# Kernel optimization log

Hardware: AMD Instinct MI355X
Metric: run time of the kernel (lower is better)

## Reference

```python
import jax, jax.numpy as jnp
import numpy as np

E, IN, H1, H2, H3, A, B = 20, 512, 1024, 512, 256, 32, 4096


def setup_inputs() -> dict:
    key = jax.random.key(0)
    ks = jax.random.split(key, 10)

    def w(k, shape, fan_in):
        return jax.random.normal(k, shape, dtype=jnp.float32) / np.sqrt(fan_in)

    return {
        "obs": jax.random.normal(ks[0], (B, IN), dtype=jnp.float32),
        # stacked expert MLP params [E, ...]
        "eW1": w(ks[1], (E, IN, H1), IN), "eb1": jnp.zeros((E, H1), jnp.float32),
        "eW2": w(ks[2], (E, H1, H2), H1), "eb2": jnp.zeros((E, H2), jnp.float32),
        "eW3": w(ks[3], (E, H2, H3), H2), "eb3": jnp.zeros((E, H3), jnp.float32),
        "eW4": w(ks[4], (E, H3, A), H3), "eb4": jnp.zeros((E, A), jnp.float32),
        # gate MLP params
        "gW1": w(ks[5], (IN, H1), IN), "gb1": jnp.zeros((H1,), jnp.float32),
        "gW2": w(ks[6], (H1, H2), H1), "gb2": jnp.zeros((H2,), jnp.float32),
        "gW3": w(ks[7], (H2, H3), H2), "gb3": jnp.zeros((H3,), jnp.float32),
        "gW4": w(ks[8], (H3, E), H3), "gb4": jnp.zeros((E,), jnp.float32),
    }


def _experts(obs, eW1, eb1, eW2, eb2, eW3, eb3, eW4, eb4):
    # batched over experts: [B, E, h]
    h = jax.nn.elu(jnp.einsum('bi,eih->beh', obs, eW1) + eb1[None])
    h = jax.nn.elu(jnp.einsum('beh,ehk->bek', h, eW2) + eb2[None])
    h = jax.nn.elu(jnp.einsum('bek,ekm->bem', h, eW3) + eb3[None])
    return jnp.einsum('bem,ema->bea', h, eW4) + eb4[None]  # [B, E, A]


def _gate(obs, gW1, gb1, gW2, gb2, gW3, gb3, gW4, gb4):
    h = jax.nn.elu(obs @ gW1 + gb1)
    h = jax.nn.elu(h @ gW2 + gb2)
    h = jax.nn.elu(h @ gW3 + gb3)
    return jax.nn.softmax(h @ gW4 + gb4, axis=-1)  # [B, E]


def reference(obs, eW1, eb1, eW2, eb2, eW3, eb3, eW4, eb4,
              gW1, gb1, gW2, gb2, gW3, gb3, gW4, gb4):
    weights = _gate(obs, gW1, gb1, gW2, gb2, gW3, gb3, gW4, gb4)       # [B, E]
    actions = _experts(obs, eW1, eb1, eW2, eb2, eW3, eb3, eW4, eb4)    # [B, E, A]
    # bmm(weights[:,None,:], actions).squeeze(1)
    return jnp.einsum('be,bea->ba', weights, actions)                   # [B, A]
```

## Files before the change

### kernel.cpp

```cpp
#include <hip/hip_runtime.h>

#define B_SZ 4096
#define E_EXP 20
#define NE 21

typedef unsigned short u16;
typedef __bf16 bf16x8 __attribute__((ext_vector_type(8)));
typedef u16 u16x8 __attribute__((ext_vector_type(8)));
typedef u16 u16x4 __attribute__((ext_vector_type(4)));
typedef float floatx4 __attribute__((ext_vector_type(4)));

static __device__ __forceinline__ u16 f2bf(float f) {
  unsigned u = __builtin_bit_cast(unsigned, f);
  u += 0x7fffu + ((u >> 16) & 1u);
  return (u16)(u >> 16);
}

static __device__ __forceinline__ bf16x8 ld_bf8(const u16* p) {
  u16x8 v = *reinterpret_cast<const u16x8*>(p);
  return __builtin_bit_cast(bf16x8, v);
}

static __device__ __forceinline__ void gld_lds16(const u16* g, u16* l) {
  __builtin_amdgcn_global_load_lds(
      (const __attribute__((address_space(1))) unsigned int*)g,
      (__attribute__((address_space(3))) unsigned int*)l, 16, 0, 0);
}


__global__ void convert_obs_kernel(const float* __restrict__ src,
                                   u16* __restrict__ dst, int n) {
  int i = (blockIdx.x * blockDim.x + threadIdx.x) * 4;
  if (i < n) {
    float4 v = *reinterpret_cast<const float4*>(src + i);
    u16x4 o;
    o.x = f2bf(v.x); o.y = f2bf(v.y); o.z = f2bf(v.z); o.w = f2bf(v.w);
    *reinterpret_cast<u16x4*>(dst + i) = o;
  }
}

__global__ void transpose_conv_kernel(const float* __restrict__ src_e,
                                      const float* __restrict__ src_g,
                                      int n_e, int K, int N, int Nout,
                                      u16* __restrict__ dst) {
  int e = blockIdx.z;
  const float* src = (e < n_e) ? (src_e + (long)e * K * N) : src_g;
  __shared__ float tile[32][33];
  int tx = threadIdx.x & 31;
  int ty = threadIdx.x >> 5;
  int kbase = blockIdx.x * 32;
  int nbase = blockIdx.y * 32;
#pragma unroll
  for (int i = 0; i < 4; ++i) {
    int k = kbase + ty + i * 8;
    int n = nbase + tx;
    float v = 0.f;
    if (k < K && n < N) v = src[(long)k * N + n];
    tile[ty + i * 8][tx] = v;
  }
  __syncthreads();
  u16* dstE = dst + (long)e * Nout * K;
#pragma unroll
  for (int i = 0; i < 4; ++i) {
    int n = nbase + ty + i * 8;
    int k = kbase + tx;
    if (n < Nout && k < K) dstE[(long)n * K + k] = f2bf(tile[tx][ty + i * 8]);
  }
}

__global__ void concat_bias_kernel(const float* __restrict__ e_b,
                                   const float* __restrict__ g_b,
                                   int E, int H, float* __restrict__ dst) {
  int i = blockIdx.x * blockDim.x + threadIdx.x;
  int total = (E + 1) * H;
  if (i < total) dst[i] = (i < E * H) ? e_b[i] : g_b[i - E * H];
}


#define BM 128
#define BN 128
#define BK 32

__global__ __launch_bounds__(256) void gemm_bias_elu_kernel(
    const u16* __restrict__ A_base, long a_estride,
    const u16* __restrict__ Wt_base, long w_estride,
    const float* __restrict__ bias_base, long b_estride,
    u16* __restrict__ C_base, long c_estride,
    int M, int N, int K) {
  int e = blockIdx.z;
  const u16* A = A_base + (long)e * a_estride;
  const u16* Wt = Wt_base + (long)e * w_estride;
  const float* bias = bias_base + (long)e * b_estride;
  u16* C = C_base + (long)e * c_estride;

  int m0 = blockIdx.y * BM;
  int n0 = blockIdx.x * BN;

  __shared__ u16 As[BM * BK];
  __shared__ u16 Bs[BN * BK];

  int tid = threadIdx.x;
  int lane = tid & 63;
  int w = tid >> 6;
  int wm = (w >> 1) * 64;
  int wn = (w & 1) * 64;
  int col = lane & 15;
  int quad = lane >> 4;

  floatx4 acc[4][4] = {};

  int srow = tid >> 2;
  int scol = (tid & 3) * 8;
  const u16* ga0 = &A[(long)(m0 + srow) * K + scol];
  const u16* ga1 = &A[(long)(m0 + 64 + srow) * K + scol];
  const u16* gb0 = &Wt[(long)(n0 + srow) * K + scol];
  const u16* gb1 = &Wt[(long)(n0 + 64 + srow) * K + scol];
  u16* la0 = &As[(size_t)tid * 8];
  u16* la1 = &As[(size_t)(256 + tid) * 8];
  u16* lb0 = &Bs[(size_t)tid * 8];
  u16* lb1 = &Bs[(size_t)(256 + tid) * 8];

  for (int k0 = 0; k0 < K; k0 += BK) {
    __syncthreads();
    gld_lds16(ga0 + k0, la0);
    gld_lds16(ga1 + k0, la1);
    gld_lds16(gb0 + k0, lb0);
    gld_lds16(gb1 + k0, lb1);
    __syncthreads();

    bf16x8 af[4], bfr[4];
#pragma unroll
    for (int t = 0; t < 4; ++t) {
      af[t] = __builtin_bit_cast(bf16x8,
          *reinterpret_cast<u16x8*>(&As[(wm + t * 16 + col) * BK + quad * 8]));
      bfr[t] = __builtin_bit_cast(bf16x8,
          *reinterpret_cast<u16x8*>(&Bs[(wn + t * 16 + col) * BK + quad * 8]));
    }
#pragma unroll
    for (int i = 0; i < 4; ++i)
#pragma unroll
      for (int j = 0; j < 4; ++j)
        acc[i][j] = __builtin_amdgcn_mfma_f32_16x16x32_bf16(af[i], bfr[j],
                                                            acc[i][j], 0, 0, 0);
  }

#pragma unroll
  for (int i = 0; i < 4; ++i) {
    int row = m0 + wm + i * 16 + quad * 4;
#pragma unroll
    for (int j = 0; j < 4; ++j) {
      int c = n0 + wn + j * 16 + col;
      float bj = bias[c];
#pragma unroll
      for (int r = 0; r < 4; ++r) {
        float v = acc[i][j][r] + bj;
        v = v > 0.f ? v : (__expf(v) - 1.f);
        C[(long)(row + r) * N + c] = f2bf(v);
      }
    }
  }
}

__global__ __launch_bounds__(64) void final_combine_kernel(
    const u16* __restrict__ h3, const u16* __restrict__ W4t,
    const u16* __restrict__ gW4t, const float* __restrict__ eb4,
    const float* __restrict__ gb4, float* __restrict__ out) {
  const int H3 = 256;
  int lane = threadIdx.x;
  int col = lane & 15;
  int quad = lane >> 4;
  int r0 = blockIdx.x * 16;

  floatx4 g0 = {}, g1 = {};
  const u16* h3g = h3 + (long)E_EXP * B_SZ * H3;
#pragma unroll
  for (int k0 = 0; k0 < 256; k0 += 32) {
    bf16x8 a = ld_bf8(&h3g[(long)(r0 + col) * H3 + k0 + quad * 8]);
    bf16x8 b0 = ld_bf8(&gW4t[(long)col * H3 + k0 + quad * 8]);
    bf16x8 b1 = ld_bf8(&gW4t[(long)(16 + col) * H3 + k0 + quad * 8]);
    g0 = __builtin_amdgcn_mfma_f32_16x16x32_bf16(a, b0, g0, 0, 0, 0);
    g1 = __builtin_amdgcn_mfma_f32_16x16x32_bf16(a, b1, g1, 0, 0, 0);
  }

  float w0[4], w1[4];
  float gbc0 = gb4[col];
  float gbc1 = (col < 4) ? gb4[16 + col] : 0.f;
#pragma unroll
  for (int r = 0; r < 4; ++r) {
    float v0 = g0[r] + gbc0;
    float v1 = (col < 4) ? (g1[r] + gbc1) : -1e30f;
    float m = fmaxf(v0, v1);
#pragma unroll
    for (int s = 1; s < 16; s <<= 1) m = fmaxf(m, __shfl_xor(m, s, 64));
    float e0 = __expf(v0 - m);
    float e1 = (col < 4) ? __expf(v1 - m) : 0.f;
    float ssum = e0 + e1;
#pragma unroll
    for (int s = 1; s < 16; s <<= 1) ssum += __shfl_xor(ssum, s, 64);
    w0[r] = e0 / ssum;
    w1[r] = e1 / ssum;
  }

  floatx4 o0 = {}, o1 = {};
  for (int e = 0; e < E_EXP; ++e) {
    floatx4 a0 = {}, a1 = {};
    const u16* he = h3 + (long)e * B_SZ * H3;
    const u16* we = W4t + (long)e * 32 * H3;
#pragma unroll
    for (int k0 = 0; k0 < 256; k0 += 32) {
      bf16x8 a = ld_bf8(&he[(long)(r0 + col) * H3 + k0 + quad * 8]);
      bf16x8 b0 = ld_bf8(&we[(long)col * H3 + k0 + quad * 8]);
      bf16x8 b1 = ld_bf8(&we[(long)(16 + col) * H3 + k0 + quad * 8]);
      a0 = __builtin_amdgcn_mfma_f32_16x16x32_bf16(a, b0, a0, 0, 0, 0);
      a1 = __builtin_amdgcn_mfma_f32_16x16x32_bf16(a, b1, a1, 0, 0, 0);
    }
    float be0 = eb4[e * 32 + col];
    float be1 = eb4[e * 32 + 16 + col];
    int src = (lane & 48) + (e & 15);
#pragma unroll
    for (int r = 0; r < 4; ++r) {
      float wr = __shfl((e < 16) ? w0[r] : w1[r], src, 64);
      o0[r] += wr * (a0[r] + be0);
      o1[r] += wr * (a1[r] + be1);
    }
  }
#pragma unroll
  for (int r = 0; r < 4; ++r) {
    int row = r0 + quad * 4 + r;
    out[(long)row * 32 + col] = o0[r];
    out[(long)row * 32 + 16 + col] = o1[r];
  }
}


static inline size_t align256(size_t x) { return (x + 255) & ~(size_t)255; }

extern "C" void kernel_launch(void* const* d_in, const int* in_sizes, int n_in,
                              void* d_out, int out_size, void* d_ws,
                              size_t ws_size, hipStream_t stream) {
  const float* obs = (const float*)d_in[0];
  const float* eW1 = (const float*)d_in[1];
  const float* eb1 = (const float*)d_in[2];
  const float* eW2 = (const float*)d_in[3];
  const float* eb2 = (const float*)d_in[4];
  const float* eW3 = (const float*)d_in[5];
  const float* eb3 = (const float*)d_in[6];
  const float* eW4 = (const float*)d_in[7];
  const float* eb4 = (const float*)d_in[8];
  const float* gW1 = (const float*)d_in[9];
  const float* gb1 = (const float*)d_in[10];
  const float* gW2 = (const float*)d_in[11];
  const float* gb2 = (const float*)d_in[12];
  const float* gW3 = (const float*)d_in[13];
  const float* gb3 = (const float*)d_in[14];
  const float* gW4 = (const float*)d_in[15];
  const float* gb4 = (const float*)d_in[16];
  float* out = (float*)d_out;
  char* ws = (char*)d_ws;

  size_t off = 0;
  size_t OFF_OBS = off;  off = align256(off + (size_t)B_SZ * 512 * 2);
  size_t OFF_W1T = off;  off = align256(off + (size_t)NE * 1024 * 512 * 2);
  size_t OFF_W2T = off;  off = align256(off + (size_t)NE * 512 * 1024 * 2);
  size_t OFF_W3T = off;  off = align256(off + (size_t)NE * 256 * 512 * 2);
  size_t OFF_W4T = off;  off = align256(off + (size_t)E_EXP * 32 * 256 * 2);
  size_t OFF_GW4T = off; off = align256(off + (size_t)32 * 256 * 2);
  size_t OFF_B1 = off;   off = align256(off + (size_t)NE * 1024 * 4);
  size_t OFF_B2 = off;   off = align256(off + (size_t)NE * 512 * 4);
  size_t OFF_B3 = off;   off = align256(off + (size_t)NE * 256 * 4);
  size_t OFF_H3 = off;   off = align256(off + (size_t)NE * B_SZ * 256 * 2);

  int chunk = B_SZ;
  size_t OFF_H1 = off;
  while (chunk > 512) {
    size_t need = (size_t)NE * chunk * 1024 * 2 + (size_t)NE * chunk * 512 * 2;
    if (OFF_H1 + need <= ws_size) break;
    chunk >>= 1;
  }
  size_t OFF_H2 = align256(OFF_H1 + (size_t)NE * chunk * 1024 * 2);

  u16* obs_bf = (u16*)(ws + OFF_OBS);
  u16* W1t = (u16*)(ws + OFF_W1T);
  u16* W2t = (u16*)(ws + OFF_W2T);
  u16* W3t = (u16*)(ws + OFF_W3T);
  u16* W4t = (u16*)(ws + OFF_W4T);
  u16* gW4t = (u16*)(ws + OFF_GW4T);
  float* b1 = (float*)(ws + OFF_B1);
  float* b2 = (float*)(ws + OFF_B2);
  float* b3 = (float*)(ws + OFF_B3);
  u16* h3 = (u16*)(ws + OFF_H3);
  u16* h1 = (u16*)(ws + OFF_H1);
  u16* h2 = (u16*)(ws + OFF_H2);

  convert_obs_kernel<<<(B_SZ * 512 / 4 + 255) / 256, 256, 0, stream>>>(
      obs, obs_bf, B_SZ * 512);
  transpose_conv_kernel<<<dim3(16, 32, NE), 256, 0, stream>>>(
      eW1, gW1, E_EXP, 512, 1024, 1024, W1t);
  transpose_conv_kernel<<<dim3(32, 16, NE), 256, 0, stream>>>(
      eW2, gW2, E_EXP, 1024, 512, 512, W2t);
  transpose_conv_kernel<<<dim3(16, 8, NE), 256, 0, stream>>>(
      eW3, gW3, E_EXP, 512, 256, 256, W3t);
  transpose_conv_kernel<<<dim3(8, 1, E_EXP), 256, 0, stream>>>(
      eW4, nullptr, E_EXP, 256, 32, 32, W4t);
  transpose_conv_kernel<<<dim3(8, 1, 1), 256, 0, stream>>>(
      gW4, nullptr, 1, 256, 20, 32, gW4t);
  concat_bias_kernel<<<(NE * 1024 + 255) / 256, 256, 0, stream>>>(
      eb1, gb1, E_EXP, 1024, b1);
  concat_bias_kernel<<<(NE * 512 + 255) / 256, 256, 0, stream>>>(
      eb2, gb2, E_EXP, 512, b2);
  concat_bias_kernel<<<(NE * 256 + 255) / 256, 256, 0, stream>>>(
      eb3, gb3, E_EXP, 256, b3);

  for (int bc = 0; bc < B_SZ; bc += chunk) {
    gemm_bias_elu_kernel<<<dim3(1024 / BN, chunk / BM, NE), 256, 0, stream>>>(
        obs_bf + (size_t)bc * 512, 0L,
        W1t, (long)1024 * 512,
        b1, 1024L,
        h1, (long)chunk * 1024, chunk, 1024, 512);
    gemm_bias_elu_kernel<<<dim3(512 / BN, chunk / BM, NE), 256, 0, stream>>>(
        h1, (long)chunk * 1024,
        W2t, (long)512 * 1024,
        b2, 512L,
        h2, (long)chunk * 512, chunk, 512, 1024);
    gemm_bias_elu_kernel<<<dim3(256 / BN, chunk / BM, NE), 256, 0, stream>>>(
        h2, (long)chunk * 512,
        W3t, (long)256 * 512,
        b3, 256L,
        h3 + (size_t)bc * 256, (long)B_SZ * 256, chunk, 256, 512);
  }

  final_combine_kernel<<<B_SZ / 16, 64, 0, stream>>>(h3, W4t, gW4t, eb4, gb4,
                                                     out);
}
```

Baseline: 575.0 us.

## Persist GEMM blocks over M tiles and vectorize transposed bias-ELU epilogue

Each GEMM block now loops over several M tiles (grid y capped at 4 or 8) so the same weight tile rows are re-read by fewer blocks and stay hot in cache. The MFMA operands are swapped so each lane holds four consecutive output columns, which lets the epilogue load the bias as a float4 and store four bf16 values at once instead of scalar strided stores. The cost is fewer blocks in flight, which can leave compute units idle on small chunks.

```diff
diff --git a/kernel.cpp b/kernel.cpp
--- a/kernel.cpp
+++ b/kernel.cpp
@@ -14,6 +14,10 @@
   unsigned u = __builtin_bit_cast(unsigned, f);
   u += 0x7fffu + ((u >> 16) & 1u);
   return (u16)(u >> 16);
+}
+
+static __device__ __forceinline__ float elu1(float v) {
+  return v > 0.f ? v : (__expf(v) - 1.f);
 }
 
 static __device__ __forceinline__ bf16x8 ld_bf8(const u16* p) {
@@ -93,7 +97,6 @@
   const float* bias = bias_base + (long)e * b_estride;
   u16* C = C_base + (long)e * c_estride;
 
-  int m0 = blockIdx.y * BM;
   int n0 = blockIdx.x * BN;
 
   __shared__ u16 As[BM * BK];
@@ -107,12 +110,8 @@
   int col = lane & 15;
   int quad = lane >> 4;
 
-  floatx4 acc[4][4] = {};
-
   int srow = tid >> 2;
   int scol = (tid & 3) * 8;
-  const u16* ga0 = &A[(long)(m0 + srow) * K + scol];
-  const u16* ga1 = &A[(long)(m0 + 64 + srow) * K + scol];
   const u16* gb0 = &Wt[(long)(n0 + srow) * K + scol];
   const u16* gb1 = &Wt[(long)(n0 + 64 + srow) * K + scol];
   u16* la0 = &As[(size_t)tid * 8];
@@ -120,42 +119,51 @@
   u16* lb0 = &Bs[(size_t)tid * 8];
   u16* lb1 = &Bs[(size_t)(256 + tid) * 8];
 
-  for (int k0 = 0; k0 < K; k0 += BK) {
-    __syncthreads();
-    gld_lds16(ga0 + k0, la0);
-    gld_lds16(ga1 + k0, la1);
-    gld_lds16(gb0 + k0, lb0);
-    gld_lds16(gb1 + k0, lb1);
-    __syncthreads();
-
-    bf16x8 af[4], bfr[4];
-#pragma unroll
-    for (int t = 0; t < 4; ++t) {
-      af[t] = __builtin_bit_cast(bf16x8,
-          *reinterpret_cast<u16x8*>(&As[(wm + t * 16 + col) * BK + quad * 8]));
-      bfr[t] = __builtin_bit_cast(bf16x8,
-          *reinterpret_cast<u16x8*>(&Bs[(wn + t * 16 + col) * BK + quad * 8]));
+  int mtiles = M / BM;
+  for (int mt = blockIdx.y; mt < mtiles; mt += gridDim.y) {
+    int m0 = mt * BM;
+    const u16* ga0 = &A[(long)(m0 + srow) * K + scol];
+    const u16* ga1 = &A[(long)(m0 + 64 + srow) * K + scol];
+
+    floatx4 acc[4][4] = {};
+
+    for (int k0 = 0; k0 < K; k0 += BK) {
+      __syncthreads();
+      gld_lds16(ga0 + k0, la0);
+      gld_lds16(ga1 + k0, la1);
+      gld_lds16(gb0 + k0, lb0);
+      gld_lds16(gb1 + k0, lb1);
+      __syncthreads();
+
+      bf16x8 xf[4], wf[4];
+#pragma unroll
+      for (int t = 0; t < 4; ++t) {
+        xf[t] = __builtin_bit_cast(bf16x8,
+            *reinterpret_cast<u16x8*>(&As[(wm + t * 16 + col) * BK + quad * 8]));
+        wf[t] = __builtin_bit_cast(bf16x8,
+            *reinterpret_cast<u16x8*>(&Bs[(wn + t * 16 + col) * BK + quad * 8]));
+      }
+#pragma unroll
+      for (int i = 0; i < 4; ++i)
+#pragma unroll
+        for (int j = 0; j < 4; ++j)
+          acc[i][j] = __builtin_amdgcn_mfma_f32_16x16x32_bf16(
+              wf[j], xf[i], acc[i][j], 0, 0, 0);
     }
-#pragma unroll
-    for (int i = 0; i < 4; ++i)
-#pragma unroll
-      for (int j = 0; j < 4; ++j)
-        acc[i][j] = __builtin_amdgcn_mfma_f32_16x16x32_bf16(af[i], bfr[j],
-                                                            acc[i][j], 0, 0, 0);
-  }
-
-#pragma unroll
-  for (int i = 0; i < 4; ++i) {
-    int row = m0 + wm + i * 16 + quad * 4;
+
 #pragma unroll
     for (int j = 0; j < 4; ++j) {
-      int c = n0 + wn + j * 16 + col;
-      float bj = bias[c];
-#pragma unroll
-      for (int r = 0; r < 4; ++r) {
-        float v = acc[i][j][r] + bj;
-        v = v > 0.f ? v : (__expf(v) - 1.f);
-        C[(long)(row + r) * N + c] = f2bf(v);
+      int nn = n0 + wn + j * 16 + quad * 4;
+      float4 b4 = *reinterpret_cast<const float4*>(&bias[nn]);
+#pragma unroll
+      for (int i = 0; i < 4; ++i) {
+        int m = m0 + wm + i * 16 + col;
+        u16x4 o;
+        o.x = f2bf(elu1(acc[i][j][0] + b4.x));
+        o.y = f2bf(elu1(acc[i][j][1] + b4.y));
+        o.z = f2bf(elu1(acc[i][j][2] + b4.z));
+        o.w = f2bf(elu1(acc[i][j][3] + b4.w));
+        *reinterpret_cast<u16x4*>(&C[(long)m * N + nn]) = o;
       }
     }
   }
@@ -311,18 +319,23 @@
   concat_bias_kernel<<<(NE * 256 + 255) / 256, 256, 0, stream>>>(
       eb3, gb3, E_EXP, 256, b3);
 
+  int mtiles = chunk / BM;
+  int ms1 = mtiles < 4 ? mtiles : 4;
+  int ms2 = mtiles < 4 ? mtiles : 4;
+  int ms3 = mtiles < 8 ? mtiles : 8;
+
   for (int bc = 0; bc < B_SZ; bc += chunk) {
-    gemm_bias_elu_kernel<<<dim3(1024 / BN, chunk / BM, NE), 256, 0, stream>>>(
+    gemm_bias_elu_kernel<<<dim3(1024 / BN, ms1, NE), 256, 0, stream>>>(
         obs_bf + (size_t)bc * 512, 0L,
         W1t, (long)1024 * 512,
         b1, 1024L,
         h1, (long)chunk * 1024, chunk, 1024, 512);
-    gemm_bias_elu_kernel<<<dim3(512 / BN, chunk / BM, NE), 256, 0, stream>>>(
+    gemm_bias_elu_kernel<<<dim3(512 / BN, ms2, NE), 256, 0, stream>>>(
         h1, (long)chunk * 1024,
         W2t, (long)512 * 1024,
         b2, 512L,
         h2, (long)chunk * 512, chunk, 512, 1024);
-    gemm_bias_elu_kernel<<<dim3(256 / BN, chunk / BM, NE), 256, 0, stream>>>(
+    gemm_bias_elu_kernel<<<dim3(256 / BN, ms3, NE), 256, 0, stream>>>(
         h2, (long)chunk * 512,
         W3t, (long)256 * 512,
         b3, 256L,
```

New measurement: 700.9 us. +21.9%, slower.
